# Optimization experiments

Measured on AMD Instinct MI355X. Metric: run time of the kernel, lower is better.

## Reference

```python
import jax, jax.numpy as jnp
import numpy as np

N, D, R, E, B = 98304, 128, 3, 491520, 16384


def setup_inputs() -> dict:
    key = jax.random.key(0)
    ks = jax.random.split(key, 12)
    s = 0.05
    return {
        "latents": jax.random.normal(ks[0], (N, D), jnp.float32),
        "Wm": jax.random.normal(ks[1], (R, D, 2 * D), jnp.float32) * s,
        "bm": jax.random.normal(ks[2], (R, D), jnp.float32) * s,
        "W1": jax.random.normal(ks[3], (D, D), jnp.float32) * s,
        "b1": jax.random.normal(ks[4], (D,), jnp.float32) * s,
        "W2": jax.random.normal(ks[5], (D, D), jnp.float32) * s,
        "b2": jax.random.normal(ks[6], (D,), jnp.float32) * s,
        "message_from": jax.random.randint(ks[7], (E,), 0, N),
        "message_to": jax.random.randint(ks[8], (E,), 0, N),
        "view_id": jax.random.randint(ks[9], (N,), 0, B),
        "ch": 6,
        "batch_size": B,
    }


def reference(latents, Wm, bm, W1, b1, W2, b2, message_from, message_to, view_id, ch, batch_size):
    # Message passing rounds: gather -> concat -> Linear+ReLU (dropout=identity in eval) -> scale -> scatter-add
    scale = 1.0 / (ch - 1)
    for r in range(Wm.shape[0]):
        h = jnp.concatenate([latents[message_from], latents[message_to]], axis=-1)  # [E, 2D]
        msg = jax.nn.relu(h @ Wm[r].T + bm[r]) * scale  # [E, D]
        latents = latents.at[message_to].add(msg)
    # Readout: sum latents per sample (note: original's `/ ch` result is discarded, so no division)
    y = jax.ops.segment_sum(latents, view_id, num_segments=batch_size)  # [B, D]
    h = jax.nn.relu(y @ W1.T + b1)
    return h @ W2.T + b2
```

## Files before the change

### kernel.cpp

```cpp
#include <hip/hip_runtime.h>

static constexpr int N  = 98304;
static constexpr int D  = 128;
static constexpr int E  = 491520;
static constexpr int B  = 16384;

using f32x4 = __attribute__((ext_vector_type(4))) float;
using s16x8 = __attribute__((ext_vector_type(8))) short;

typedef __attribute__((address_space(3))) void lds_void;
typedef const __attribute__((address_space(1))) void gbl_void;

__device__ __forceinline__ ushort f2bf(float x) {
    unsigned u = __float_as_uint(x);
    return (ushort)((u + 0x7fffu + ((u >> 16) & 1u)) >> 16);
}
__device__ __forceinline__ float bflo(unsigned u) { return __uint_as_float(u << 16); }
__device__ __forceinline__ float bfhi(unsigned u) { return __uint_as_float(u & 0xffff0000u); }

__global__ void zero2_kernel(int* __restrict__ p) {
    int i = blockIdx.x * 256 + threadIdx.x;
    if (i < N + B) p[i] = 0;
}

__global__ void hist2_kernel(const int* __restrict__ eto, const int* __restrict__ view,
                             int* __restrict__ cnt, int* __restrict__ vcnt) {
    int gid = blockIdx.x * 256 + threadIdx.x;
    if (gid < E) atomicAdd(&cnt[eto[gid]], 1);
    else if (gid < E + N) atomicAdd(&vcnt[view[gid - E]], 1);
}

__global__ __launch_bounds__(256) void scan1_kernel(const int* __restrict__ cnt, int* __restrict__ excl,
                                                    const int* __restrict__ vcnt, int* __restrict__ vexcl,
                                                    int* __restrict__ bsum) {
    __shared__ int s[256];
    const int b = blockIdx.x, t = threadIdx.x;
    const int* src; int* dst; int base;
    if (b < 96) { src = cnt;  dst = excl;  base = b * 1024 + t * 4; }
    else        { src = vcnt; dst = vexcl; base = (b - 96) * 1024 + t * 4; }
    int4 v = *reinterpret_cast<const int4*>(src + base);
    int local = v.x + v.y + v.z + v.w;
    s[t] = local; __syncthreads();
    for (int off = 1; off < 256; off <<= 1) {
        int x = (t >= off) ? s[t - off] : 0;
        __syncthreads();
        s[t] += x;
        __syncthreads();
    }
    int excl_t = s[t] - local;
    if (t == 255) bsum[b] = s[t];
    int4 o;
    o.x = excl_t; o.y = o.x + v.x; o.z = o.y + v.y; o.w = o.z + v.z;
    *reinterpret_cast<int4*>(dst + base) = o;
}

__global__ __launch_bounds__(128) void scan2_kernel(int* __restrict__ bsum) {
    __shared__ int s[128];
    const int t = threadIdx.x;
    int val = (t < 112) ? bsum[t] : 0;
    s[t] = val;
    __syncthreads();
    #pragma unroll
    for (int off = 1; off < 128; off <<= 1) {
        int x = (t >= off) ? s[t - off] : 0;
        __syncthreads();
        s[t] += x;
        __syncthreads();
    }
    int incl = s[t];
    int seg0_total = s[95];
    int excl = incl - val;
    if (t < 96) bsum[t] = excl;
    else if (t < 112) bsum[t] = excl - seg0_total;
}

__global__ void scan3_kernel(int* __restrict__ excl, int* __restrict__ vexcl,
                             const int* __restrict__ bsum) {
    int b = blockIdx.x, t = threadIdx.x;
    if (b < 384) { int i = b * 256 + t; excl[i] += bsum[i >> 10]; }
    else         { int i = (b - 384) * 256 + t; vexcl[i] += bsum[96 + (i >> 10)]; }
}

__global__ void scatter2_kernel(const int* __restrict__ efrom, const int* __restrict__ eto,
                                const int* __restrict__ view,
                                int* __restrict__ ecur, int* __restrict__ vcur,
                                int* __restrict__ sfrom, int* __restrict__ perm) {
    int gid = blockIdx.x * 256 + threadIdx.x;
    if (gid < E) {
        int p = atomicAdd(&ecur[eto[gid]], 1);
        sfrom[p] = efrom[gid];
    } else if (gid < E + N) {
        int n = gid - E;
        int p = atomicAdd(&vcur[view[n]], 1);
        perm[p] = n;
    }
}

__global__ void convUV_kernel(const float* __restrict__ Wm, ushort* __restrict__ Wf) {
    int gid = blockIdx.x * 256 + threadIdx.x;
    if (gid >= 3 * 32768) return;
    int r = gid >> 15, rem = gid & 32767;
    int j = rem & 7, lane = (rem >> 3) & 63, grp = rem >> 9;
    int kt = grp >> 4, nt = grp & 15;
    int n = (nt & 7) * 16 + (lane & 15);
    int k = kt * 32 + (lane >> 4) * 8 + j;
    int col = ((nt >> 3) << 7) + k;
    Wf[gid] = f2bf(Wm[((size_t)r * 128 + n) * 256 + col]);
}

__global__ void convW12_kernel(const float* __restrict__ W1, const float* __restrict__ W2,
                               ushort* __restrict__ Wb12) {
    int gid = blockIdx.x * 256 + threadIdx.x;
    if (gid >= 2 * 16384) return;
    int w = gid >> 14, rem = gid & 16383;
    int n = rem >> 7, k = rem & 127;
    int kt = k >> 5, nt = n >> 4;
    int lane = (n & 15) + (((k >> 3) & 3) << 4);
    int j = k & 7;
    const float* W = w ? W2 : W1;
    Wb12[w * 16384 + ((kt * 8 + nt) * 64 + lane) * 8 + j] = f2bf(W[rem]);
}

__global__ __launch_bounds__(512) void uv_kernel(
    const float* __restrict__ Asrc, ushort* __restrict__ Z,
    const ushort* __restrict__ Wft, const float* __restrict__ bm_r)
{
    __shared__ alignas(16) ushort wlds[32768];
    const int t = threadIdx.x;

    #pragma unroll
    for (int it = 0; it < 8; ++it) {
        int idx = t + it * 512;
        __builtin_amdgcn_global_load_lds((gbl_void*)(Wft + idx * 8),
                                         (lds_void*)(wlds + idx * 8), 16, 0, 0);
    }

    const int wave = t >> 6, lane = t & 63;
    const int col16 = lane & 15, kq = lane >> 4;
    const int arow = blockIdx.x * 128 + wave * 16 + col16;

    const float4* Ar = reinterpret_cast<const float4*>(Asrc + (size_t)arow * 128);
    float4 areg[8];
    #pragma unroll
    for (int kt = 0; kt < 4; ++kt) {
        areg[2 * kt]     = Ar[kt * 8 + kq * 2];
        areg[2 * kt + 1] = Ar[kt * 8 + kq * 2 + 1];
    }

    f32x4 acc[16];
    #pragma unroll
    for (int nt = 0; nt < 16; ++nt) acc[nt] = (f32x4){0.f, 0.f, 0.f, 0.f};

    __syncthreads();

    const char* wb = reinterpret_cast<const char*>(wlds);
    #pragma unroll
    for (int kt = 0; kt < 4; ++kt) {
        float4 a0 = areg[2 * kt], a1 = areg[2 * kt + 1];
        union { s16x8 v; ushort u[8]; } pk;
        pk.u[0] = f2bf(a0.x); pk.u[1] = f2bf(a0.y); pk.u[2] = f2bf(a0.z); pk.u[3] = f2bf(a0.w);
        pk.u[4] = f2bf(a1.x); pk.u[5] = f2bf(a1.y); pk.u[6] = f2bf(a1.z); pk.u[7] = f2bf(a1.w);
        #pragma unroll
        for (int nt = 0; nt < 16; ++nt) {
            s16x8 wfr = *reinterpret_cast<const s16x8*>(wb + (((kt * 16 + nt) * 64 + lane) << 4));
            acc[nt] = __builtin_amdgcn_mfma_f32_16x16x32_bf16(wfr, pk.v, acc[nt], 0, 0, 0);
        }
    }

    ushort* zr = Z + (size_t)arow * 256;
    #pragma unroll
    for (int nt = 0; nt < 16; ++nt) {
        float4 bq;
        if (nt >= 8) bq = *reinterpret_cast<const float4*>(bm_r + (nt - 8) * 16 + kq * 4);
        else         bq = (float4){0.f, 0.f, 0.f, 0.f};
        union { uint2 d; ushort u[4]; } pk4;
        pk4.u[0] = f2bf(acc[nt][0] + bq.x);
        pk4.u[1] = f2bf(acc[nt][1] + bq.y);
        pk4.u[2] = f2bf(acc[nt][2] + bq.z);
        pk4.u[3] = f2bf(acc[nt][3] + bq.w);
        int cbase = ((nt >> 3) << 7) + (nt & 7) * 16 + kq * 4;
        *reinterpret_cast<uint2*>(zr + cbase) = pk4.d;
    }
}

__global__ __launch_bounds__(256) void edge_sum_kernel(
    const ushort* __restrict__ Z, const float* __restrict__ Lsrc, float* __restrict__ Ldst,
    const int* __restrict__ sfrom, const int* __restrict__ ends, const int* __restrict__ ch_ptr)
{
    const int t = threadIdx.x;
    const int wave = t >> 6, lane = t & 63;
    const float scale = 1.0f / (float)(ch_ptr[0] - 1);
    const int v0 = blockIdx.x * 16 + wave * 4;

    int bnd[5];
    bnd[0] = (v0 == 0) ? 0 : ends[v0 - 1];
    #pragma unroll
    for (int i = 0; i < 4; ++i) bnd[i + 1] = ends[v0 + i];

    unsigned vv[4]; float2 lold[4];
    #pragma unroll
    for (int i = 0; i < 4; ++i) {
        vv[i] = *reinterpret_cast<const unsigned*>(Z + (size_t)(v0 + i) * 256 + 128 + lane * 2);
        lold[i] = *reinterpret_cast<const float2*>(Lsrc + (size_t)(v0 + i) * 128 + lane * 2);
    }

    const int cmax = bnd[4] - 1;

    int idx[4][8];
    #pragma unroll
    for (int i = 0; i < 4; ++i) {
        #pragma unroll
        for (int k = 0; k < 8; ++k) {
            int c = bnd[i] + k;
            c = (c > cmax) ? cmax : c;
            c = (c < 0) ? 0 : c;
            idx[i][k] = sfrom[c];
        }
    }

    unsigned u[4][8];
    #pragma unroll
    for (int i = 0; i < 4; ++i) {
        #pragma unroll
        for (int k = 0; k < 8; ++k)
            u[i][k] = *reinterpret_cast<const unsigned*>(Z + (size_t)idx[i][k] * 256 + lane * 2);
    }

    float A0[4], A1[4];
    #pragma unroll
    for (int i = 0; i < 4; ++i) { A0[i] = 0.f; A1[i] = 0.f; }
    #pragma unroll
    for (int i = 0; i < 4; ++i) {
        const float vl = bflo(vv[i]), vh = bfhi(vv[i]);
        #pragma unroll
        for (int k = 0; k < 8; ++k) {
            float m = (bnd[i] + k < bnd[i + 1]) ? 1.f : 0.f;
            A0[i] += m * fmaxf(bflo(u[i][k]) + vl, 0.f);
            A1[i] += m * fmaxf(bfhi(u[i][k]) + vh, 0.f);
        }
    }

    #pragma unroll
    for (int i = 0; i < 4; ++i) {
        const float vl = bflo(vv[i]), vh = bfhi(vv[i]);
        for (int e = bnd[i] + 8; e < bnd[i + 1]; ++e) {
            int f = sfrom[e];
            unsigned uu = *reinterpret_cast<const unsigned*>(Z + (size_t)f * 256 + lane * 2);
            A0[i] += fmaxf(bflo(uu) + vl, 0.f);
            A1[i] += fmaxf(bfhi(uu) + vh, 0.f);
        }
    }

    #pragma unroll
    for (int i = 0; i < 4; ++i) {
        float2 o;
        o.x = lold[i].x + scale * A0[i];
        o.y = lold[i].y + scale * A1[i];
        *reinterpret_cast<float2*>(Ldst + (size_t)(v0 + i) * 128 + lane * 2) = o;
    }
}

__global__ __launch_bounds__(256) void segsum_sorted_kernel(
    const float* __restrict__ L, const int* __restrict__ perm,
    const int* __restrict__ vends, float* __restrict__ y)
{
    const int t = threadIdx.x;
    const int wave = t >> 6, lane = t & 63;
    const int v = blockIdx.x * 4 + wave;
    const int lo = (v == 0) ? 0 : vends[v - 1];
    const int hi = vends[v];

    float a0 = 0.f, a1 = 0.f;
    for (int e = lo; e < hi; e += 2) {
        int last = hi - 1;
        int e1 = (e + 1 < hi) ? e + 1 : last;
        float m1 = (e + 1 < hi) ? 1.f : 0.f;
        int n0 = perm[e], n1 = perm[e1];
        float2 x0 = *reinterpret_cast<const float2*>(L + (size_t)n0 * 128 + lane * 2);
        float2 x1 = *reinterpret_cast<const float2*>(L + (size_t)n1 * 128 + lane * 2);
        a0 += x0.x + m1 * x1.x;
        a1 += x0.y + m1 * x1.y;
    }
    float2 o; o.x = a0; o.y = a1;
    *reinterpret_cast<float2*>(y + (size_t)v * 128 + lane * 2) = o;
}

__global__ __launch_bounds__(256) void readout_mfma_kernel(
    const float* __restrict__ y, float* __restrict__ outp,
    const ushort* __restrict__ Wb1, const ushort* __restrict__ Wb2,
    const float* __restrict__ b1, const float* __restrict__ b2)
{
    __shared__ alignas(16) ushort hs[64 * 128];
    const int t = threadIdx.x;
    const int r0 = blockIdx.x * 64;
    char* hbase = reinterpret_cast<char*>(hs);
    const float4* y4 = reinterpret_cast<const float4*>(y);

    #pragma unroll
    for (int it = 0; it < 4; ++it) {
        int c = t + it * 256;
        int e = c >> 4, p = c & 15;
        int g = p ^ (e & 15);
        float4 a = y4[(size_t)(r0 + e) * 32 + g * 2];
        float4 bq = y4[(size_t)(r0 + e) * 32 + g * 2 + 1];
        union { s16x8 v; ushort u[8]; } pk;
        pk.u[0] = f2bf(a.x); pk.u[1] = f2bf(a.y); pk.u[2] = f2bf(a.z); pk.u[3] = f2bf(a.w);
        pk.u[4] = f2bf(bq.x); pk.u[5] = f2bf(bq.y); pk.u[6] = f2bf(bq.z); pk.u[7] = f2bf(bq.w);
        *reinterpret_cast<s16x8*>(hbase + e * 256 + p * 16) = pk.v;
    }
    __syncthreads();

    const int wave = t >> 6, lane = t & 63;
    const int rrow = wave * 16 + (lane & 15);
    const int kq = lane >> 4;
    const int rx = rrow & 15;
    const char* hrow = hbase + rrow * 256;
    const int col16 = lane & 15;

    f32x4 acc[8];
    #pragma unroll
    for (int nt = 0; nt < 8; ++nt) acc[nt] = (f32x4){0.f, 0.f, 0.f, 0.f};
    const s16x8* wf1 = reinterpret_cast<const s16x8*>(Wb1);
    #pragma unroll
    for (int kt = 0; kt < 4; ++kt) {
        int C = kt * 4 + kq;
        s16x8 a = *reinterpret_cast<const s16x8*>(hrow + ((C ^ rx) & 15) * 16);
        #pragma unroll
        for (int nt = 0; nt < 8; ++nt)
            acc[nt] = __builtin_amdgcn_mfma_f32_16x16x32_bf16(a, wf1[(kt * 8 + nt) * 64 + lane], acc[nt], 0, 0, 0);
    }
    __syncthreads();

    #pragma unroll
    for (int nt = 0; nt < 8; ++nt) {
        float bias = b1[nt * 16 + col16];
        #pragma unroll
        for (int j = 0; j < 4; ++j) {
            int r = wave * 16 + (lane >> 4) * 4 + j;
            float h = fmaxf(acc[nt][j] + bias, 0.f);
            int colfull = nt * 16 + col16;
            int chunk = colfull >> 3;
            int bo = ((chunk ^ (r & 15)) * 16) + (colfull & 7) * 2;
            *reinterpret_cast<ushort*>(hbase + r * 256 + bo) = f2bf(h);
        }
    }
    __syncthreads();

    f32x4 acc2[8];
    #pragma unroll
    for (int nt = 0; nt < 8; ++nt) acc2[nt] = (f32x4){0.f, 0.f, 0.f, 0.f};
    const s16x8* wf2 = reinterpret_cast<const s16x8*>(Wb2);
    #pragma unroll
    for (int kt = 0; kt < 4; ++kt) {
        int C = kt * 4 + kq;
        s16x8 a = *reinterpret_cast<const s16x8*>(hrow + ((C ^ rx) & 15) * 16);
        #pragma unroll
        for (int nt = 0; nt < 8; ++nt)
            acc2[nt] = __builtin_amdgcn_mfma_f32_16x16x32_bf16(a, wf2[(kt * 8 + nt) * 64 + lane], acc2[nt], 0, 0, 0);
    }

    #pragma unroll
    for (int nt = 0; nt < 8; ++nt) {
        float bias = b2[nt * 16 + col16];
        #pragma unroll
        for (int j = 0; j < 4; ++j) {
            int r = r0 + wave * 16 + (lane >> 4) * 4 + j;
            outp[(size_t)r * 128 + nt * 16 + col16] = acc2[nt][j] + bias;
        }
    }
}

extern "C" void kernel_launch(void* const* d_in, const int* in_sizes, int n_in,
                              void* d_out, int out_size, void* d_ws, size_t ws_size,
                              hipStream_t stream) {
    const float* latents = (const float*)d_in[0];
    const float* Wm      = (const float*)d_in[1];
    const float* bm      = (const float*)d_in[2];
    const float* W1      = (const float*)d_in[3];
    const float* b1      = (const float*)d_in[4];
    const float* W2      = (const float*)d_in[5];
    const float* b2      = (const float*)d_in[6];
    const int*   efrom   = (const int*)d_in[7];
    const int*   eto     = (const int*)d_in[8];
    const int*   view    = (const int*)d_in[9];
    const int*   ch      = (const int*)d_in[10];

    float*  L  = (float*)d_ws;
    ushort* Z  = (ushort*)(L + (size_t)N * D);
    float*  yb = (float*)Z;
    ushort* Wb12 = (ushort*)((char*)Z + 8388608);

    char* ob = (char*)d_out;
    ushort* WUVf = (ushort*)ob;
    int* cnt   = (int*)(ob + 196608);
    int* vcnt  = cnt + N;
    int* excl  = vcnt + B;
    int* vexcl = excl + N;
    int* bsum  = vexcl + B;
    int* sfrom = bsum + 128;
    int* perm  = sfrom + E;
    float* outp = (float*)d_out;

    convUV_kernel<<<384, 256, 0, stream>>>(Wm, WUVf);
    zero2_kernel<<<(N + B) / 256, 256, 0, stream>>>(cnt);
    hist2_kernel<<<(E + N) / 256, 256, 0, stream>>>(eto, view, cnt, vcnt);
    scan1_kernel<<<112, 256, 0, stream>>>(cnt, excl, vcnt, vexcl, bsum);
    scan2_kernel<<<1, 128, 0, stream>>>(bsum);
    scan3_kernel<<<448, 256, 0, stream>>>(excl, vexcl, bsum);
    scatter2_kernel<<<(E + N) / 256, 256, 0, stream>>>(efrom, eto, view, excl, vexcl, sfrom, perm);

    uv_kernel<<<N / 128, 512, 0, stream>>>(latents, Z, WUVf, bm);
    edge_sum_kernel<<<N / 16, 256, 0, stream>>>(Z, latents, L, sfrom, excl, ch);
    uv_kernel<<<N / 128, 512, 0, stream>>>(L, Z, WUVf + 32768, bm + D);
    edge_sum_kernel<<<N / 16, 256, 0, stream>>>(Z, L, L, sfrom, excl, ch);
    uv_kernel<<<N / 128, 512, 0, stream>>>(L, Z, WUVf + 65536, bm + 2 * D);
    edge_sum_kernel<<<N / 16, 256, 0, stream>>>(Z, L, L, sfrom, excl, ch);

    convW12_kernel<<<128, 256, 0, stream>>>(W1, W2, Wb12);
    segsum_sorted_kernel<<<B / 4, 256, 0, stream>>>(L, perm, vexcl, yb);
    readout_mfma_kernel<<<B / 64, 256, 0, stream>>>(yb, outp, Wb12, Wb12 + 16384, b1, b2);
}
```

Baseline: 303.4 us.

## Pad per-node edge lists to multiples of four with sentinel row

Rounds each destination node's incoming edge count up to a multiple of four in the CSR scan and fills the padding slots with a sentinel index N. The sentinel points at a Z row of bf16 negative infinity, so ReLU turns those contributions into zero. The edge-sum kernel then drops masking and clamping, prefetches four edges per node instead of eight, and walks the tail in unmasked groups of four loads. This cuts predication and per-edge loop overhead and raises memory-level parallelism in the tail. In exchange it does extra padded gathers, adds two small setup kernels, and relies on the sentinel row fitting in workspace past Z.

```diff
diff --git a/kernel.cpp b/kernel.cpp
--- a/kernel.cpp
+++ b/kernel.cpp
@@ -36,9 +36,11 @@
     __shared__ int s[256];
     const int b = blockIdx.x, t = threadIdx.x;
     const int* src; int* dst; int base;
-    if (b < 96) { src = cnt;  dst = excl;  base = b * 1024 + t * 4; }
-    else        { src = vcnt; dst = vexcl; base = (b - 96) * 1024 + t * 4; }
+    bool pad = (b < 96);
+    if (pad) { src = cnt;  dst = excl;  base = b * 1024 + t * 4; }
+    else     { src = vcnt; dst = vexcl; base = (b - 96) * 1024 + t * 4; }
     int4 v = *reinterpret_cast<const int4*>(src + base);
+    if (pad) { v.x = (v.x + 3) & ~3; v.y = (v.y + 3) & ~3; v.z = (v.z + 3) & ~3; v.w = (v.w + 3) & ~3; }
     int local = v.x + v.y + v.z + v.w;
     s[t] = local; __syncthreads();
     for (int off = 1; off < 256; off <<= 1) {
@@ -96,6 +98,17 @@
     }
 }
 
+__global__ void fillpad_kernel(const int* __restrict__ cur, int* __restrict__ sfrom) {
+    int v = blockIdx.x * 256 + threadIdx.x;
+    if (v >= N) return;
+    int c = cur[v], e = (c + 3) & ~3;
+    for (; c < e; ++c) sfrom[c] = N;
+}
+
+__global__ void sentinel_kernel(ushort* __restrict__ Z) {
+    Z[(size_t)N * 256 + threadIdx.x] = 0xFF80;
+}
+
 __global__ void convUV_kernel(const float* __restrict__ Wm, ushort* __restrict__ Wf) {
     int gid = blockIdx.x * 256 + threadIdx.x;
     if (gid >= 3 * 32768) return;
@@ -193,9 +206,9 @@
     const int v0 = blockIdx.x * 16 + wave * 4;
 
     int bnd[5];
-    bnd[0] = (v0 == 0) ? 0 : ends[v0 - 1];
-    #pragma unroll
-    for (int i = 0; i < 4; ++i) bnd[i + 1] = ends[v0 + i];
+    bnd[0] = (v0 == 0) ? 0 : ((ends[v0 - 1] + 3) & ~3);
+    #pragma unroll
+    for (int i = 0; i < 4; ++i) bnd[i + 1] = (ends[v0 + i] + 3) & ~3;
 
     unsigned vv[4]; float2 lold[4];
     #pragma unroll
@@ -204,58 +217,45 @@
         lold[i] = *reinterpret_cast<const float2*>(Lsrc + (size_t)(v0 + i) * 128 + lane * 2);
     }
 
-    const int cmax = bnd[4] - 1;
-
-    int idx[4][8];
+    int idx[4][4];
     #pragma unroll
     for (int i = 0; i < 4; ++i) {
         #pragma unroll
-        for (int k = 0; k < 8; ++k) {
+        for (int k = 0; k < 4; ++k) {
             int c = bnd[i] + k;
-            c = (c > cmax) ? cmax : c;
-            c = (c < 0) ? 0 : c;
-            idx[i][k] = sfrom[c];
-        }
-    }
-
-    unsigned u[4][8];
-    #pragma unroll
-    for (int i = 0; i < 4; ++i) {
-        #pragma unroll
-        for (int k = 0; k < 8; ++k)
+            idx[i][k] = (c < bnd[i + 1]) ? sfrom[c] : N;
+        }
+    }
+    unsigned u[4][4];
+    #pragma unroll
+    for (int i = 0; i < 4; ++i)
+        #pragma unroll
+        for (int k = 0; k < 4; ++k)
             u[i][k] = *reinterpret_cast<const unsigned*>(Z + (size_t)idx[i][k] * 256 + lane * 2);
-    }
-
-    float A0[4], A1[4];
-    #pragma unroll
-    for (int i = 0; i < 4; ++i) { A0[i] = 0.f; A1[i] = 0.f; }
+
     #pragma unroll
     for (int i = 0; i < 4; ++i) {
         const float vl = bflo(vv[i]), vh = bfhi(vv[i]);
-        #pragma unroll
-        for (int k = 0; k < 8; ++k) {
-            float m = (bnd[i] + k < bnd[i + 1]) ? 1.f : 0.f;
-            A0[i] += m * fmaxf(bflo(u[i][k]) + vl, 0.f);
-            A1[i] += m * fmaxf(bfhi(u[i][k]) + vh, 0.f);
-        }
-    }
-
-    #pragma unroll
-    for (int i = 0; i < 4; ++i) {
-        const float vl = bflo(vv[i]), vh = bfhi(vv[i]);
-        for (int e = bnd[i] + 8; e < bnd[i + 1]; ++e) {
-            int f = sfrom[e];
-            unsigned uu = *reinterpret_cast<const unsigned*>(Z + (size_t)f * 256 + lane * 2);
-            A0[i] += fmaxf(bflo(uu) + vl, 0.f);
-            A1[i] += fmaxf(bfhi(uu) + vh, 0.f);
-        }
-    }
-
-    #pragma unroll
-    for (int i = 0; i < 4; ++i) {
+        float a0 = 0.f, a1 = 0.f;
+        #pragma unroll
+        for (int k = 0; k < 4; ++k) {
+            a0 += fmaxf(bflo(u[i][k]) + vl, 0.f);
+            a1 += fmaxf(bfhi(u[i][k]) + vh, 0.f);
+        }
+        for (int e = bnd[i] + 4; e < bnd[i + 1]; e += 4) {
+            int f0 = sfrom[e], f1 = sfrom[e + 1], f2 = sfrom[e + 2], f3 = sfrom[e + 3];
+            unsigned w0 = *reinterpret_cast<const unsigned*>(Z + (size_t)f0 * 256 + lane * 2);
+            unsigned w1 = *reinterpret_cast<const unsigned*>(Z + (size_t)f1 * 256 + lane * 2);
+            unsigned w2 = *reinterpret_cast<const unsigned*>(Z + (size_t)f2 * 256 + lane * 2);
+            unsigned w3 = *reinterpret_cast<const unsigned*>(Z + (size_t)f3 * 256 + lane * 2);
+            a0 += fmaxf(bflo(w0) + vl, 0.f) + fmaxf(bflo(w1) + vl, 0.f)
+                + fmaxf(bflo(w2) + vl, 0.f) + fmaxf(bflo(w3) + vl, 0.f);
+            a1 += fmaxf(bfhi(w0) + vh, 0.f) + fmaxf(bfhi(w1) + vh, 0.f)
+                + fmaxf(bfhi(w2) + vh, 0.f) + fmaxf(bfhi(w3) + vh, 0.f);
+        }
         float2 o;
-        o.x = lold[i].x + scale * A0[i];
-        o.y = lold[i].y + scale * A1[i];
+        o.x = lold[i].x + scale * a0;
+        o.y = lold[i].y + scale * a1;
         *reinterpret_cast<float2*>(Ldst + (size_t)(v0 + i) * 128 + lane * 2) = o;
     }
 }
@@ -398,7 +398,7 @@
     int* vexcl = excl + N;
     int* bsum  = vexcl + B;
     int* sfrom = bsum + 128;
-    int* perm  = sfrom + E;
+    int* perm  = sfrom + E + 3 * N;
     float* outp = (float*)d_out;
 
     convUV_kernel<<<384, 256, 0, stream>>>(Wm, WUVf);
@@ -408,6 +408,8 @@
     scan2_kernel<<<1, 128, 0, stream>>>(bsum);
     scan3_kernel<<<448, 256, 0, stream>>>(excl, vexcl, bsum);
     scatter2_kernel<<<(E + N) / 256, 256, 0, stream>>>(efrom, eto, view, excl, vexcl, sfrom, perm);
+    fillpad_kernel<<<N / 256, 256, 0, stream>>>(excl, sfrom);
+    sentinel_kernel<<<1, 256, 0, stream>>>(Z);
 
     uv_kernel<<<N / 128, 512, 0, stream>>>(latents, Z, WUVf, bm);
     edge_sum_kernel<<<N / 16, 256, 0, stream>>>(Z, latents, L, sfrom, excl, ch);
```

Result: no change. 309.2 us (+1.9%).
